# Kernel optimization log

Hardware: AMD Instinct MI355X
Metric: run time of the kernel (lower is better)

The kernel has to match this reference:

```python
import jax, jax.numpy as jnp
import numpy as np

TOP_K = 25
END_K = 25
TEMP = 0.07
CON_RATE = 0.1
NUM_LABELS = 2
NEG_INF = -1e30  # stand-in for -inf that keeps softmax/topk well-behaved


def _l2norm(x):
    return x / jnp.sqrt(jnp.sum(x * x, axis=-1, keepdims=True))


def _head(x, dense_w, dense_b, out_w, out_b):
    # dropout is identity in eval mode
    h = jnp.tanh(x @ dense_w + dense_b)
    return h @ out_w + out_b


def _ce(logits, targets):
    lp = jax.nn.log_softmax(logits, axis=-1)
    return -jnp.take_along_axis(lp, targets[:, None], axis=1).mean()


def setup_inputs() -> dict:
    key = jax.random.key(0)
    ks = jax.random.split(key, 10)
    B, K, H = 128, 32768, 768
    fq = jax.random.normal(ks[2], (K, H), dtype=jnp.float32)
    # buffer init in torch: F.normalize(feature_queue, dim=0)
    fq = fq / jnp.linalg.norm(fq, axis=0, keepdims=True)
    s = 0.02
    return {
        "pooled": jax.random.normal(ks[0], (B, H), dtype=jnp.float32),
        "labels": jax.random.randint(ks[1], (B,), 0, NUM_LABELS),
        "feature_queue": fq,
        "label_queue": jax.random.randint(ks[3], (K,), 0, NUM_LABELS),
        "cls_dense_w": s * jax.random.normal(ks[4], (H, H), dtype=jnp.float32),
        "cls_dense_b": jnp.zeros((H,), jnp.float32),
        "cls_out_w": s * jax.random.normal(ks[5], (H, NUM_LABELS), dtype=jnp.float32),
        "cls_out_b": jnp.zeros((NUM_LABELS,), jnp.float32),
        "con_dense_w": s * jax.random.normal(ks[6], (H, H), dtype=jnp.float32),
        "con_dense_b": jnp.zeros((H,), jnp.float32),
        "con_out_w": s * jax.random.normal(ks[7], (H, H), dtype=jnp.float32),
        "con_out_b": jnp.zeros((H,), jnp.float32),
    }


def _select_pos_neg(liner_q, labels, feature_queue, label_queue, pos_min, neg_min):
    # cos_sim: [B, K]  (einsum 'nc,kc->nk'; queue rows are detached)
    cos_sim = jnp.einsum("nc,kc->nk", liner_q, feature_queue)
    pos_mask = labels[:, None] == label_queue[None, :]  # [B, K] bool
    pos_sample = jnp.where(pos_mask, cos_sim, NEG_INF)
    neg_sample = jnp.where(pos_mask, NEG_INF, cos_sim)
    pos_top, _ = jax.lax.top_k(pos_sample, pos_min)   # [B, pos_min]
    neg_top, _ = jax.lax.top_k(neg_sample, neg_min)   # [B, neg_min]
    pos = jnp.concatenate([pos_top[:, :TOP_K], pos_top[:, -END_K:]], axis=-1)
    pos = pos.reshape(-1, 1)                                   # [B*(TOP_K+END_K), 1]
    neg = jnp.tile(neg_top, (1, TOP_K + END_K)).reshape(-1, neg_min)
    return jnp.concatenate([pos, neg], axis=-1) / TEMP


def reference(pooled, labels, feature_queue, label_queue,
              cls_dense_w, cls_dense_b, cls_out_w, cls_out_b,
              con_dense_w, con_dense_b, con_out_w, con_out_b):
    # data-dependent top-k sizes (concrete int labels -> static sizes)
    pm = np.asarray(labels)[:, None] == np.asarray(label_queue)[None, :]
    pos_min = int(pm.sum(-1).min())
    neg_min = int((~pm).sum(-1).min())

    logits_cls = _head(pooled, cls_dense_w, cls_dense_b, cls_out_w, cls_out_b)
    loss_cls = _ce(logits_cls, labels)

    liner_q = _l2norm(_head(pooled, con_dense_w, con_dense_b, con_out_w, con_out_b))
    logits_con = _select_pos_neg(liner_q, labels, jax.lax.stop_gradient(feature_queue),
                                 label_queue, pos_min, neg_min)
    labels_con = jnp.zeros((logits_con.shape[0],), jnp.int32)
    loss_con = _ce(logits_con, labels_con)

    loss = loss_con * CON_RATE + loss_cls * (1.0 - CON_RATE)
    return loss
```

## Files before the change

### kernel.cpp

```cpp
#include <hip/hip_runtime.h>
#include <math.h>

#define BB 128
#define HH 768
#define KQ 32768
#define PCAP 18432
#define NB 4096
#define CCAP 512

constexpr float TINV = 1.0f / 0.07f;

typedef __attribute__((ext_vector_type(8))) short short8;
typedef __attribute__((ext_vector_type(4))) float f32x4;
typedef __attribute__((address_space(3))) void lds_void;
typedef const __attribute__((address_space(1))) void gbl_void;

__device__ __forceinline__ unsigned short f2bf(float f) {
  unsigned u = __float_as_uint(f);
  unsigned r = u + 0x7FFFu + ((u >> 16) & 1u);
  return (unsigned short)(r >> 16);
}
__device__ __forceinline__ float bf2f(unsigned short h) {
  return __uint_as_float(((unsigned)h) << 16);
}
__device__ __forceinline__ unsigned cvtpk(float a, float b) {
  unsigned r;
  asm("v_cvt_pk_bf16_f32 %0, %1, %2" : "=v"(r) : "v"(a), "v"(b));
  return r;
}
__device__ __forceinline__ unsigned f2key(float f) {
  unsigned u = __float_as_uint(f);
  return u ^ (unsigned)(((int)u >> 31) | 0x80000000);
}
__device__ __forceinline__ float key2f(unsigned k) {
  unsigned u = (k & 0x80000000u) ? (k & 0x7FFFFFFFu) : ~k;
  return __uint_as_float(u);
}
__device__ __forceinline__ unsigned long long shfl_down_u64(unsigned long long v, int o) {
  unsigned lo = (unsigned)v, hi = (unsigned)(v >> 32);
  lo = __shfl_down(lo, o);
  hi = __shfl_down(hi, o);
  return ((unsigned long long)hi << 32) | lo;
}
__device__ __forceinline__ void gl16(const unsigned short* g, unsigned short* l) {
  __builtin_amdgcn_global_load_lds((gbl_void*)g, (lds_void*)l, 16, 0, 0);
}

__global__ __launch_bounds__(256) void prep_kernel(
    const float* __restrict__ W0, const float* __restrict__ W1,
    const float* __restrict__ W2, const float* __restrict__ pooled,
    unsigned short* __restrict__ Wt0, unsigned short* __restrict__ Wt1,
    unsigned short* __restrict__ Wt2, unsigned short* __restrict__ pooledb,
    float* __restrict__ out) {
  const int bid = blockIdx.x, tid = threadIdx.x;
  if (bid == 0 && tid == 0) out[0] = 0.0f;
  if (bid < 432) {
    const float* W = (bid < 144) ? W0 : (bid < 288 ? W1 : W2);
    unsigned short* Wt = (bid < 144) ? Wt0 : (bid < 288 ? Wt1 : Wt2);
    const int t = bid % 144;
    const int k0 = (t / 12) * 64, n0 = (t % 12) * 64;
    __shared__ float Ls[64][65];
    const int r = tid >> 4, c4 = (tid & 15) * 4;
#pragma unroll
    for (int i = 0; i < 4; ++i) {
      const int rr = r + i * 16;
      const float4 v = *reinterpret_cast<const float4*>(W + (size_t)(k0 + rr) * HH + n0 + c4);
      Ls[rr][c4 + 0] = v.x; Ls[rr][c4 + 1] = v.y;
      Ls[rr][c4 + 2] = v.z; Ls[rr][c4 + 3] = v.w;
    }
    __syncthreads();
#pragma unroll
    for (int i = 0; i < 4; ++i) {
      const int rn = r + i * 16;
      ushort4 o;
      o.x = f2bf(Ls[c4 + 0][rn]);
      o.y = f2bf(Ls[c4 + 1][rn]);
      o.z = f2bf(Ls[c4 + 2][rn]);
      o.w = f2bf(Ls[c4 + 3][rn]);
      *reinterpret_cast<ushort4*>(Wt + (size_t)(n0 + rn) * HH + k0 + c4) = o;
    }
  } else {
    const int idx = (bid - 432) * 1024 + tid * 4;
    const float4 v = *reinterpret_cast<const float4*>(pooled + idx);
    ushort4 o;
    o.x = f2bf(v.x); o.y = f2bf(v.y); o.z = f2bf(v.z); o.w = f2bf(v.w);
    *reinterpret_cast<ushort4*>(pooledb + idx) = o;
  }
}

__device__ __forceinline__ void head_core(
    unsigned short (*Abuf)[128 * 64], const unsigned short* __restrict__ Ab,
    const unsigned short* __restrict__ Wt, const float* __restrict__ bias,
    unsigned short* __restrict__ Out, bool do_tanh, int q0, int tid) {
  const int lane = tid & 63, wid = tid >> 6;
  const int a_r = lane & 15, a_kq = lane >> 4;
  int asrc[4], adst[4];
#pragma unroll
  for (int j = 0; j < 4; ++j) {
    const int rr = (wid * 4 + j) * 8 + (lane >> 3);
    const int kb = (lane & 7) ^ (rr & 7);
    asrc[j] = rr * HH + kb * 8;
    adst[j] = (wid * 4 + j) * 512;
  }
  const int bn = q0 + wid * 16 + a_r;
  const unsigned short* __restrict__ bptr = Wt + (size_t)bn * HH + a_kq * 8;
  int aslot[2];
#pragma unroll
  for (int st = 0; st < 2; ++st) aslot[st] = (((st * 4 + a_kq) ^ (a_r & 7)) << 3);

  f32x4 acc[8];
#pragma unroll
  for (int m = 0; m < 8; ++m) acc[m] = (f32x4){0.f, 0.f, 0.f, 0.f};

#pragma unroll
  for (int j = 0; j < 4; ++j) gl16(Ab + asrc[j], &Abuf[0][adst[j]]);
  __builtin_amdgcn_sched_barrier(0);
#pragma unroll
  for (int j = 0; j < 4; ++j) gl16(Ab + 64 + asrc[j], &Abuf[1][adst[j]]);
  __builtin_amdgcn_sched_barrier(0);
  short8 bv[4];
#pragma unroll
  for (int p = 0; p < 4; ++p)
    bv[p] = *reinterpret_cast<const short8*>(bptr + p * 32);
  __builtin_amdgcn_sched_barrier(0);
  asm volatile("s_waitcnt vmcnt(8)" ::: "memory");
  __builtin_amdgcn_s_barrier();
  __builtin_amdgcn_sched_barrier(0);

#pragma unroll
  for (int c = 0; c < 12; ++c) {
    if (c + 2 < 12) {
#pragma unroll
      for (int j = 0; j < 4; ++j)
        gl16(Ab + (c + 2) * 64 + asrc[j], &Abuf[(c + 2) % 3][adst[j]]);
    }
    __builtin_amdgcn_sched_barrier(0);
    const unsigned short* __restrict__ Abc = Abuf[c % 3];
#pragma unroll
    for (int st = 0; st < 2; ++st) {
      const int s = c * 2 + st;
      const short8 bb = bv[s & 3];
      if (s + 4 < 24)
        bv[s & 3] = *reinterpret_cast<const short8*>(bptr + (s + 4) * 32);
      const int sl = aslot[st];
#pragma unroll
      for (int m = 0; m < 8; ++m) {
        const short8 aa =
            *reinterpret_cast<const short8*>(&Abc[(m * 16 + a_r) * 64 + sl]);
        acc[m] = __builtin_amdgcn_mfma_f32_16x16x32_bf16(aa, bb, acc[m], 0, 0, 0);
      }
    }
    if (c < 11) {
      __builtin_amdgcn_sched_barrier(0);
      if (c == 0)       asm volatile("s_waitcnt vmcnt(10)" ::: "memory");
      else if (c <= 9)  asm volatile("s_waitcnt vmcnt(8)" ::: "memory");
      else              asm volatile("s_waitcnt vmcnt(2)" ::: "memory");
      __builtin_amdgcn_s_barrier();
      __builtin_amdgcn_sched_barrier(0);
    }
  }

  const float bvl = bias[bn];
#pragma unroll
  for (int m = 0; m < 8; ++m)
#pragma unroll
    for (int r = 0; r < 4; ++r) {
      float v = acc[m][r] + bvl;
      if (do_tanh) v = tanhf(v);
      Out[(size_t)(m * 16 + a_kq * 4 + r) * HH + bn] = f2bf(v);
    }
}

__global__ __launch_bounds__(256) void heads_mfma(
    const unsigned short* __restrict__ pooledb,
    const unsigned short* __restrict__ Wt0, const float* __restrict__ b0,
    unsigned short* __restrict__ H1b,
    const unsigned short* __restrict__ Wt1, const float* __restrict__ b1,
    unsigned short* __restrict__ H2b) {
  __shared__ unsigned short Abuf[3][128 * 64];
  const int z = blockIdx.x / 12;
  const int q0 = (blockIdx.x % 12) * 64;
  head_core(Abuf, pooledb, z ? Wt1 : Wt0, z ? b1 : b0, z ? H2b : H1b, true, q0,
            threadIdx.x);
}

__global__ __launch_bounds__(256) void out_gemm(
    const unsigned short* __restrict__ H2b, const unsigned short* __restrict__ Wt2,
    const float* __restrict__ b2v, unsigned short* __restrict__ Yb) {
  __shared__ unsigned short Abuf[3][128 * 64];
  head_core(Abuf, H2b, Wt2, b2v, Yb, false, blockIdx.x * 64, threadIdx.x);
}

__global__ __launch_bounds__(256, 2) void cos_gemm_mfma(
    const unsigned short* __restrict__ qh, const float* __restrict__ FQ,
    unsigned short* __restrict__ Cb) {
  __shared__ unsigned short Abuf[4][128 * 64];
  const int tid = threadIdx.x;
  const int lane = tid & 63, wid = tid >> 6;
  const int bid = blockIdx.x;
  const int swz = (bid & 7) * 64 + (bid >> 3);
  const int q0 = swz * 64;
  const int a_r = lane & 15, a_kq = lane >> 4;

  int asrc[4], adst[4];
#pragma unroll
  for (int j = 0; j < 4; ++j) {
    const int rr = (wid * 4 + j) * 8 + (lane >> 3);
    const int kb = (lane & 7) ^ (rr & 7);
    asrc[j] = rr * HH + kb * 8;
    adst[j] = (wid * 4 + j) * 512;
  }
  const float* __restrict__ bptr = FQ + (size_t)(q0 + wid * 16 + a_r) * HH + a_kq * 8;
  int aslot[2];
#pragma unroll
  for (int st = 0; st < 2; ++st) aslot[st] = (((st * 4 + a_kq) ^ (a_r & 7)) << 3);

  f32x4 acc[8];
#pragma unroll
  for (int m = 0; m < 8; ++m) acc[m] = (f32x4){0.f, 0.f, 0.f, 0.f};

#pragma unroll
  for (int j = 0; j < 4; ++j) gl16(qh + asrc[j], &Abuf[0][adst[j]]);
  __builtin_amdgcn_sched_barrier(0);
#pragma unroll
  for (int j = 0; j < 4; ++j) gl16(qh + 64 + asrc[j], &Abuf[1][adst[j]]);
  __builtin_amdgcn_sched_barrier(0);
#pragma unroll
  for (int j = 0; j < 4; ++j) gl16(qh + 128 + asrc[j], &Abuf[2][adst[j]]);
  __builtin_amdgcn_sched_barrier(0);
  float4 bv[8][2];
#pragma unroll
  for (int p = 0; p < 8; ++p) {
    bv[p][0] = *reinterpret_cast<const float4*>(bptr + p * 32);
    bv[p][1] = *reinterpret_cast<const float4*>(bptr + p * 32 + 4);
  }
  __builtin_amdgcn_sched_barrier(0);
  asm volatile("s_waitcnt vmcnt(24)" ::: "memory");
  __builtin_amdgcn_s_barrier();
  __builtin_amdgcn_sched_barrier(0);

#pragma unroll
  for (int c = 0; c < 12; ++c) {
    if (c + 3 < 12) {
#pragma unroll
      for (int j = 0; j < 4; ++j)
        gl16(qh + (c + 3) * 64 + asrc[j], &Abuf[(c + 3) & 3][adst[j]]);
    }
    __builtin_amdgcn_sched_barrier(0);
    const unsigned short* __restrict__ Ab = Abuf[c & 3];
#pragma unroll
    for (int st = 0; st < 2; ++st) {
      const int s = c * 2 + st;
      const float4 v0 = bv[s & 7][0], v1 = bv[s & 7][1];
      if (s + 8 < 24) {
        bv[s & 7][0] = *reinterpret_cast<const float4*>(bptr + (s + 8) * 32);
        bv[s & 7][1] = *reinterpret_cast<const float4*>(bptr + (s + 8) * 32 + 4);
      }
      union { short8 s8; unsigned u[4]; } cb;
      cb.u[0] = cvtpk(v0.x, v0.y);
      cb.u[1] = cvtpk(v0.z, v0.w);
      cb.u[2] = cvtpk(v1.x, v1.y);
      cb.u[3] = cvtpk(v1.z, v1.w);
      const short8 bb = cb.s8;
      const int sl = aslot[st];
#pragma unroll
      for (int m = 0; m < 8; ++m) {
        const short8 aa =
            *reinterpret_cast<const short8*>(&Ab[(m * 16 + a_r) * 64 + sl]);
        acc[m] = __builtin_amdgcn_mfma_f32_16x16x32_bf16(aa, bb, acc[m], 0, 0, 0);
      }
    }
    if (c < 11) {
      __builtin_amdgcn_sched_barrier(0);
      if (c == 0)      asm volatile("s_waitcnt vmcnt(28)" ::: "memory");
      else if (c == 1) asm volatile("s_waitcnt vmcnt(32)" ::: "memory");
      else if (c <= 7) asm volatile("s_waitcnt vmcnt(20)" ::: "memory");
      else if (c == 8) asm volatile("s_waitcnt vmcnt(16)" ::: "memory");
      else if (c == 9) asm volatile("s_waitcnt vmcnt(8)" ::: "memory");
      else             asm volatile("s_waitcnt vmcnt(0)" ::: "memory");
      __builtin_amdgcn_s_barrier();
      __builtin_amdgcn_sched_barrier(0);
    }
  }

  const int ccol = q0 + wid * 16 + a_r;
#pragma unroll
  for (int m = 0; m < 8; ++m)
#pragma unroll
    for (int r = 0; r < 4; ++r)
      Cb[(size_t)(m * 16 + a_kq * 4 + r) * KQ + ccol] = f2bf(acc[m][r]);
}

__global__ __launch_bounds__(1024) void select_kernel(
    const unsigned short* __restrict__ Cb, const unsigned short* __restrict__ Yb,
    const unsigned short* __restrict__ H1b, const float* __restrict__ W2,
    const float* __restrict__ cb2, const int* __restrict__ labels,
    const int* __restrict__ lq, float* __restrict__ out) {
  const int b = blockIdx.x;
  const int tid = threadIdx.x;
  const int lane = tid & 63, wid = tid >> 6;
  const unsigned short* __restrict__ row = Cb + (size_t)b * KQ;
  const int lab = labels[b];

  __shared__ __align__(16) unsigned poskeys[PCAP];
  __shared__ unsigned hist[NB + 1];
  __shared__ unsigned cand[3][CCAP];
  __shared__ int candn[3];
  __shared__ float redm[16], reds[16], redmin[16], redmax[16];
  __shared__ int redn[16];
  __shared__ unsigned wsum[16];
  __shared__ float shc0[16], shc1[16];
  __shared__ int abin[3], acnt[3];
  __shared__ unsigned akey[3];
  __shared__ unsigned long long accg;
  __shared__ float gs0, gsm, s_logE, s_vmin, s_vmax, s_rs;
  __shared__ float ssq[2];
  __shared__ int s_cnt, s_m, has01;

  if (tid == 0) { s_cnt = 0; gs0 = 0.f; gsm = 0.f; accg = 0ull; has01 = 0; }
  if (tid < 3) candn[tid] = 0;

  float cp0 = 0.f, cp1 = 0.f;
  if (tid < HH) {
    const float v = bf2f(H1b[(size_t)b * HH + tid]);
    cp0 = v * W2[tid * 2 + 0];
    cp1 = v * W2[tid * 2 + 1];
  }
#pragma unroll
  for (int o = 32; o; o >>= 1) {
    cp0 += __shfl_down(cp0, o);
    cp1 += __shfl_down(cp1, o);
  }
  if (lane == 0) { shc0[wid] = cp0; shc1[wid] = cp1; }

  float ssl = 0.f;
  if (tid < 96) {
    const short8 y8 =
        *reinterpret_cast<const short8*>(Yb + (size_t)b * HH + tid * 8);
#pragma unroll
    for (int e = 0; e < 8; ++e) {
      const float v = bf2f((unsigned short)y8[e]);
      ssl = fmaf(v, v, ssl);
    }
  }
#pragma unroll
  for (int o = 32; o; o >>= 1) ssl += __shfl_down(ssl, o);
  if (lane == 0 && wid < 2) ssq[wid] = ssl;
  __syncthreads();
  if (tid == 0) s_rs = rsqrtf(ssq[0] + ssq[1]);
  __syncthreads();
  const float rs = s_rs;

  const int base = tid << 5;
  unsigned qm = 0u;
  {
    const int4* __restrict__ lq4 = reinterpret_cast<const int4*>(lq + base);
#pragma unroll
    for (int u = 0; u < 8; ++u) {
      const int4 q = lq4[u];
      qm |= (unsigned)(q.x != 0) << (u * 4 + 0);
      qm |= (unsigned)(q.y != 0) << (u * 4 + 1);
      qm |= (unsigned)(q.z != 0) << (u * 4 + 2);
      qm |= (unsigned)(q.w != 0) << (u * 4 + 3);
    }
  }
  if (tid < BB) atomicOr(&has01, 1 << labels[tid]);
  const unsigned pmask = lab ? qm : ~qm;
  float va[32];
#pragma unroll
  for (int u = 0; u < 4; ++u) {
    const short8 y8 = *reinterpret_cast<const short8*>(row + base + (u << 3));
#pragma unroll
    for (int e = 0; e < 8; ++e)
      va[(u << 3) + e] = bf2f((unsigned short)y8[e]) * rs;
  }
  float mneg = -3.0e38f, sneg = 0.f, vmin = 3.0e38f, vmax = -3.0e38f;
#pragma unroll
  for (int j = 0; j < 32; ++j) {
    if ((pmask >> j) & 1u) {
      vmin = fminf(vmin, va[j]);
      vmax = fmaxf(vmax, va[j]);
    } else {
      mneg = fmaxf(mneg, va[j] * TINV);
    }
  }
#pragma unroll
  for (int j = 0; j < 32; ++j) {
    if (!((pmask >> j) & 1u)) sneg += __expf(va[j] * TINV - mneg);
  }
  int nc = __popc(qm);
#pragma unroll
  for (int o = 32; o; o >>= 1) {
    const float mo = __shfl_down(mneg, o), so = __shfl_down(sneg, o);
    const float M = fmaxf(mneg, mo);
    sneg = sneg * __expf(mneg - M) + so * __expf(mo - M);
    mneg = M;
    vmin = fminf(vmin, __shfl_down(vmin, o));
    vmax = fmaxf(vmax, __shfl_down(vmax, o));
    nc += __shfl_down(nc, o);
  }
  if (lane == 0) {
    redm[wid] = mneg; reds[wid] = sneg; redmin[wid] = vmin; redmax[wid] = vmax;
    redn[wid] = nc;
  }

  const int np = __popc(pmask);
  unsigned incl = (unsigned)np;
#pragma unroll
  for (int o = 1; o < 64; o <<= 1) {
    const unsigned t = __shfl_up(incl, o);
    if (lane >= o) incl += t;
  }
  const unsigned excl = incl - (unsigned)np;
  const unsigned wtot = __shfl(incl, 63);
  unsigned wbase = 0u;
  if (lane == 63) wbase = (unsigned)atomicAdd(&s_cnt, (int)wtot);
  wbase = __shfl(wbase, 63);
  const int ofs = (int)(wbase + excl);
  if (ofs + np <= PCAP) {
#pragma unroll
    for (int j = 0; j < 32; ++j) {
      if ((pmask >> j) & 1u)
        poskeys[ofs + __popc(pmask & ((1u << j) - 1u))] = f2key(va[j]);
    }
  }
  __syncthreads();

  const int P = s_cnt;
  if (tid == 0) {
    float M = redm[0], S = 0.f;
    float mn = redmin[0], mx = redmax[0];
    int n1 = 0;
    for (int w = 1; w < 16; ++w) {
      M = fmaxf(M, redm[w]);
      mn = fminf(mn, redmin[w]);
      mx = fmaxf(mx, redmax[w]);
    }
    for (int w = 0; w < 16; ++w) { S += reds[w] * __expf(redm[w] - M); n1 += redn[w]; }
    s_logE = M + logf(S);
    s_vmin = mn;
    s_vmax = mx;
    int mm = 0x7fffffff;
    if (has01 & 1) mm = min(mm, KQ - n1);
    if (has01 & 2) mm = min(mm, n1);
    s_m = mm;
  }
  if (tid < ((4 - (P & 3)) & 3)) poskeys[P + tid] = 0u;
  for (int i = tid; i < NB + 1; i += 1024) hist[i] = 0u;
  __syncthreads();

  const float cE = s_logE;
  const int m = s_m;
  const float vmn = s_vmin;
  const float scale = (float)NB * (1.0f - 1e-6f) / fmaxf(s_vmax - vmn, 1e-30f);
  auto key2bin = [&](unsigned k) {
    int bn = (int)((key2f(k) - vmn) * scale);
    return bn < 0 ? 0 : (bn > NB - 1 ? NB - 1 : bn);
  };

  for (int i = tid; i < P; i += 1024) atomicAdd(&hist[key2bin(poskeys[i])], 1u);
  __syncthreads();

  const int t4 = tid << 2;
  const unsigned h0 = hist[t4], h1 = hist[t4 + 1], h2 = hist[t4 + 2], h3 = hist[t4 + 3];
  const unsigned part = h0 + h1 + h2 + h3;
  unsigned sinc = part;
#pragma unroll
  for (int o = 1; o < 64; o <<= 1) {
    const unsigned t = __shfl_up(sinc, o);
    if (lane >= o) sinc += t;
  }
  if (lane == 63) wsum[wid] = sinc;
  __syncthreads();
  unsigned woff = 0;
  for (int w = 0; w < wid; ++w) woff += wsum[w];
  const unsigned exb = woff + sinc - part;
  hist[t4] = exb; hist[t4 + 1] = exb + h0; hist[t4 + 2] = exb + h0 + h1;
  hist[t4 + 3] = exb + h0 + h1 + h2;
  if (tid == 1023) hist[NB] = exb + part;
  __syncthreads();

  const int rt0 = 25, rt1 = m - 25, rt2 = m;
  const unsigned idx0 = (unsigned)(P - rt0), idx1 = (unsigned)(P - rt1), idx2 = (unsigned)(P - rt2);
#pragma unroll
  for (int i = 0; i < 4; ++i) {
    const int bb = t4 + i;
    const unsigned pb = hist[bb], pb1 = hist[bb + 1];
    if (pb <= idx0 && idx0 < pb1) { abin[0] = bb; acnt[0] = P - (int)pb1; }
    if (pb <= idx1 && idx1 < pb1) { abin[1] = bb; acnt[1] = P - (int)pb1; }
    if (pb <= idx2 && idx2 < pb1) { abin[2] = bb; acnt[2] = P - (int)pb1; }
  }
  __syncthreads();

  const int tb0 = abin[0], tb1 = abin[1], tb2 = abin[2];
  for (int i = tid; i < P; i += 1024) {
    const unsigned k = poskeys[i];
    const int bn = key2bin(k);
    if (bn == tb0) { const int p = atomicAdd(&candn[0], 1); if (p < CCAP) cand[0][p] = k; }
    if (bn == tb1) { const int p = atomicAdd(&candn[1], 1); if (p < CCAP) cand[1][p] = k; }
    if (bn == tb2) { const int p = atomicAdd(&candn[2], 1); if (p < CCAP) cand[2][p] = k; }
  }
  __syncthreads();

  if (wid < 3) {
    const int j = wid;
    const int rts[3] = {rt0, rt1, rt2};
    const int cnt = candn[j] < CCAP ? candn[j] : CCAP;
    const int rr = rts[j] - acnt[j];
    for (int i = lane; i < cnt; i += 64) {
      const unsigned k = cand[j][i];
      int gt = 0, eq = 0;
      for (int q = 0; q < cnt; ++q) {
        const unsigned kq = cand[j][q];
        gt += (kq > k);
        eq += (kq == k);
      }
      if (gt < rr && rr <= gt + eq) akey[j] = k;
    }
  }
  __syncthreads();

  const unsigned a0 = akey[0], a1 = akey[1], a2 = akey[2];
  const int P4c = (P + 3) >> 2;
  const uint4* __restrict__ pk4 = reinterpret_cast<const uint4*>(poskeys);

  float s0 = 0.f, sm = 0.f;
  unsigned q0c = 0, q1c = 0, q2c = 0;
  for (int i = tid; i < P4c; i += 1024) {
    const uint4 kv = pk4[i];
    const unsigned ks[4] = {kv.x, kv.y, kv.z, kv.w};
#pragma unroll
    for (int j = 0; j < 4; ++j) {
      const unsigned k = ks[j];
      if (k > a2) {
        ++q2c;
        const bool top = (k > a0), mid = (k <= a1);
        if (k > a1) ++q1c;
        if (top) ++q0c;
        if (top || mid) {
          const float a = key2f(k) * TINV;
          const float d = cE - a;
          const float fv = fmaxf(d, 0.f) + log1pf(__expf(-fabsf(d)));
          if (top) s0 += fv;
          if (mid) sm += fv;
        }
      }
    }
  }
  unsigned long long pc = (unsigned long long)q0c |
                          ((unsigned long long)q1c << 20) |
                          ((unsigned long long)q2c << 40);
#pragma unroll
  for (int o = 32; o; o >>= 1) {
    s0 += __shfl_down(s0, o);
    sm += __shfl_down(sm, o);
    pc += shfl_down_u64(pc, o);
  }
  if (lane == 0) {
    atomicAdd(&gs0, s0);
    atomicAdd(&gsm, sm);
    atomicAdd(&accg, pc);
  }
  __syncthreads();
  if (tid == 0) {
    const unsigned long long t = accg;
    const float C0 = (float)(unsigned)(t & 0xFFFFFu);
    const float C1 = (float)(unsigned)((t >> 20) & 0xFFFFFu);
    const float C2 = (float)(unsigned)((t >> 40) & 0xFFFFFu);
    auto fval = [&](unsigned kk) {
      const float a = key2f(kk) * TINV;
      const float d = cE - a;
      return fmaxf(d, 0.f) + log1pf(__expf(-fabsf(d)));
    };
    const float f0 = fval(a0), f1 = fval(a1), f2 = fval(a2);
    const float top25 = gs0 + (25.0f - C0) * f0;
    const float mid = gsm + ((float)m - C2) * f2 - ((float)(m - 25) - C1) * f1;
    float l0 = cb2[0], l1 = cb2[1];
    for (int w = 0; w < 16; ++w) { l0 += shc0[w]; l1 += shc1[w]; }
    const float mx = fmaxf(l0, l1), mn = fminf(l0, l1);
    const float lse = mx + log1pf(__expf(mn - mx));
    const float ce = lse - (lab ? l1 : l0);
    atomicAdd(out, 0.9f * ce * (1.0f / 128.0f) +
                       0.1f * (top25 + mid) * (1.0f / 6400.0f));
  }
}

extern "C" void kernel_launch(void* const* d_in, const int* in_sizes, int n_in,
                              void* d_out, int out_size, void* d_ws, size_t ws_size,
                              hipStream_t stream) {
  const float* pooled = (const float*)d_in[0];
  const int* labels = (const int*)d_in[1];
  const float* fq = (const float*)d_in[2];
  const int* lq = (const int*)d_in[3];
  const float* cls_dw = (const float*)d_in[4];
  const float* cls_db = (const float*)d_in[5];
  const float* cls_ow = (const float*)d_in[6];
  const float* cls_ob = (const float*)d_in[7];
  const float* con_dw = (const float*)d_in[8];
  const float* con_db = (const float*)d_in[9];
  const float* con_ow = (const float*)d_in[10];
  const float* con_ob = (const float*)d_in[11];
  float* out = (float*)d_out;

  float* ws = (float*)d_ws;
  unsigned short* Cb = (unsigned short*)ws;
  unsigned short* Yb = Cb + (size_t)BB * KQ;
  unsigned short* H1b = Yb + 98304;
  unsigned short* H2b = H1b + 98304;
  unsigned short* pooledb = H2b + 98304;
  unsigned short* Wt0 = Cb;
  unsigned short* Wt1 = Wt0 + 589824;
  unsigned short* Wt2 = Wt1 + 589824;

  prep_kernel<<<528, 256, 0, stream>>>(cls_dw, con_dw, con_ow, pooled,
                                       Wt0, Wt1, Wt2, pooledb, out);
  heads_mfma<<<24, 256, 0, stream>>>(pooledb, Wt0, cls_db, H1b,
                                     Wt1, con_db, H2b);
  out_gemm<<<12, 256, 0, stream>>>(H2b, Wt2, con_ob, Yb);
  cos_gemm_mfma<<<512, 256, 0, stream>>>(Yb, fq, Cb);
  select_kernel<<<128, 1024, 0, stream>>>(Cb, Yb, H1b, cls_ow, cls_ob,
                                          labels, lq, out);
}
```

Before: 81.57 us.

## Retile head GEMMs to 64x128 tiles with full-K LDS preload

```diff
diff --git a/kernel.cpp b/kernel.cpp
--- a/kernel.cpp
+++ b/kernel.cpp
@@ -88,87 +88,70 @@
   }
 }
 
-__device__ __forceinline__ void head_core(
-    unsigned short (*Abuf)[128 * 64], const unsigned short* __restrict__ Ab,
+__device__ __forceinline__ void head2_core(
+    unsigned short (*Al)[64 * 64], const unsigned short* __restrict__ A,
     const unsigned short* __restrict__ Wt, const float* __restrict__ bias,
-    unsigned short* __restrict__ Out, bool do_tanh, int q0, int tid) {
+    unsigned short* __restrict__ Out, bool do_tanh, int r0, int n0, int tid) {
   const int lane = tid & 63, wid = tid >> 6;
   const int a_r = lane & 15, a_kq = lane >> 4;
-  int asrc[4], adst[4];
-#pragma unroll
-  for (int j = 0; j < 4; ++j) {
-    const int rr = (wid * 4 + j) * 8 + (lane >> 3);
+
+  int asrc[2], adst[2];
+#pragma unroll
+  for (int j = 0; j < 2; ++j) {
+    const int rr = wid * 16 + j * 8 + (lane >> 3);
     const int kb = (lane & 7) ^ (rr & 7);
-    asrc[j] = rr * HH + kb * 8;
-    adst[j] = (wid * 4 + j) * 512;
-  }
-  const int bn = q0 + wid * 16 + a_r;
-  const unsigned short* __restrict__ bptr = Wt + (size_t)bn * HH + a_kq * 8;
+    asrc[j] = (r0 + rr) * HH + kb * 8;
+    adst[j] = (wid * 16 + j * 8) * 64;
+  }
+#pragma unroll
+  for (int c = 0; c < 12; ++c)
+#pragma unroll
+    for (int j = 0; j < 2; ++j)
+      gl16(A + c * 64 + asrc[j], &Al[c][adst[j]]);
+  asm volatile("s_waitcnt vmcnt(0)" ::: "memory");
+  __builtin_amdgcn_s_barrier();
+
+  const unsigned short* __restrict__ bp0 =
+      Wt + (size_t)(n0 + wid * 32 + a_r) * HH + a_kq * 8;
+  const unsigned short* __restrict__ bp1 = bp0 + (size_t)16 * HH;
   int aslot[2];
 #pragma unroll
   for (int st = 0; st < 2; ++st) aslot[st] = (((st * 4 + a_kq) ^ (a_r & 7)) << 3);
 
-  f32x4 acc[8];
-#pragma unroll
-  for (int m = 0; m < 8; ++m) acc[m] = (f32x4){0.f, 0.f, 0.f, 0.f};
-
-#pragma unroll
-  for (int j = 0; j < 4; ++j) gl16(Ab + asrc[j], &Abuf[0][adst[j]]);
-  __builtin_amdgcn_sched_barrier(0);
-#pragma unroll
-  for (int j = 0; j < 4; ++j) gl16(Ab + 64 + asrc[j], &Abuf[1][adst[j]]);
-  __builtin_amdgcn_sched_barrier(0);
-  short8 bv[4];
-#pragma unroll
-  for (int p = 0; p < 4; ++p)
-    bv[p] = *reinterpret_cast<const short8*>(bptr + p * 32);
-  __builtin_amdgcn_sched_barrier(0);
-  asm volatile("s_waitcnt vmcnt(8)" ::: "memory");
-  __builtin_amdgcn_s_barrier();
-  __builtin_amdgcn_sched_barrier(0);
-
-#pragma unroll
-  for (int c = 0; c < 12; ++c) {
-    if (c + 2 < 12) {
-#pragma unroll
-      for (int j = 0; j < 4; ++j)
-        gl16(Ab + (c + 2) * 64 + asrc[j], &Abuf[(c + 2) % 3][adst[j]]);
-    }
-    __builtin_amdgcn_sched_barrier(0);
-    const unsigned short* __restrict__ Abc = Abuf[c % 3];
-#pragma unroll
-    for (int st = 0; st < 2; ++st) {
-      const int s = c * 2 + st;
-      const short8 bb = bv[s & 3];
-      if (s + 4 < 24)
-        bv[s & 3] = *reinterpret_cast<const short8*>(bptr + (s + 4) * 32);
-      const int sl = aslot[st];
-#pragma unroll
-      for (int m = 0; m < 8; ++m) {
-        const short8 aa =
-            *reinterpret_cast<const short8*>(&Abc[(m * 16 + a_r) * 64 + sl]);
-        acc[m] = __builtin_amdgcn_mfma_f32_16x16x32_bf16(aa, bb, acc[m], 0, 0, 0);
+  f32x4 acc[4][2];
+#pragma unroll
+  for (int m = 0; m < 4; ++m)
+#pragma unroll
+    for (int n = 0; n < 2; ++n) acc[m][n] = (f32x4){0.f, 0.f, 0.f, 0.f};
+
+#pragma unroll
+  for (int s = 0; s < 24; ++s) {
+    const short8 b0 = *reinterpret_cast<const short8*>(bp0 + s * 32);
+    const short8 b1 = *reinterpret_cast<const short8*>(bp1 + s * 32);
+    const int c = s >> 1;
+    const int sl = aslot[s & 1];
+#pragma unroll
+    for (int m = 0; m < 4; ++m) {
+      const short8 aa =
+          *reinterpret_cast<const short8*>(&Al[c][(m * 16 + a_r) * 64 + sl]);
+      acc[m][0] = __builtin_amdgcn_mfma_f32_16x16x32_bf16(aa, b0, acc[m][0], 0, 0, 0);
+      acc[m][1] = __builtin_amdgcn_mfma_f32_16x16x32_bf16(aa, b1, acc[m][1], 0, 0, 0);
+    }
+  }
+
+#pragma unroll
+  for (int n = 0; n < 2; ++n) {
+    const int col = n0 + wid * 32 + n * 16 + a_r;
+    const float bvl = bias[col];
+#pragma unroll
+    for (int m = 0; m < 4; ++m)
+#pragma unroll
+      for (int r = 0; r < 4; ++r) {
+        float v = acc[m][n][r] + bvl;
+        if (do_tanh) v = tanhf(v);
+        Out[(size_t)(r0 + m * 16 + a_kq * 4 + r) * HH + col] = f2bf(v);
       }
-    }
-    if (c < 11) {
-      __builtin_amdgcn_sched_barrier(0);
-      if (c == 0)       asm volatile("s_waitcnt vmcnt(10)" ::: "memory");
-      else if (c <= 9)  asm volatile("s_waitcnt vmcnt(8)" ::: "memory");
-      else              asm volatile("s_waitcnt vmcnt(2)" ::: "memory");
-      __builtin_amdgcn_s_barrier();
-      __builtin_amdgcn_sched_barrier(0);
-    }
-  }
-
-  const float bvl = bias[bn];
-#pragma unroll
-  for (int m = 0; m < 8; ++m)
-#pragma unroll
-    for (int r = 0; r < 4; ++r) {
-      float v = acc[m][r] + bvl;
-      if (do_tanh) v = tanhf(v);
-      Out[(size_t)(m * 16 + a_kq * 4 + r) * HH + bn] = f2bf(v);
-    }
+  }
 }
 
 __global__ __launch_bounds__(256) void heads_mfma(
@@ -177,18 +160,18 @@
     unsigned short* __restrict__ H1b,
     const unsigned short* __restrict__ Wt1, const float* __restrict__ b1,
     unsigned short* __restrict__ H2b) {
-  __shared__ unsigned short Abuf[3][128 * 64];
-  const int z = blockIdx.x / 12;
-  const int q0 = (blockIdx.x % 12) * 64;
-  head_core(Abuf, pooledb, z ? Wt1 : Wt0, z ? b1 : b0, z ? H2b : H1b, true, q0,
-            threadIdx.x);
+  __shared__ unsigned short Al[12][64 * 64];
+  const int z = blockIdx.z;
+  head2_core(Al, pooledb, z ? Wt1 : Wt0, z ? b1 : b0, z ? H2b : H1b, true,
+             blockIdx.y * 64, blockIdx.x * 128, threadIdx.x);
 }
 
 __global__ __launch_bounds__(256) void out_gemm(
     const unsigned short* __restrict__ H2b, const unsigned short* __restrict__ Wt2,
     const float* __restrict__ b2v, unsigned short* __restrict__ Yb) {
-  __shared__ unsigned short Abuf[3][128 * 64];
-  head_core(Abuf, H2b, Wt2, b2v, Yb, false, blockIdx.x * 64, threadIdx.x);
+  __shared__ unsigned short Al[12][64 * 64];
+  head2_core(Al, H2b, Wt2, b2v, Yb, false, blockIdx.y * 64, blockIdx.x * 128,
+             threadIdx.x);
 }
 
 __global__ __launch_bounds__(256, 2) void cos_gemm_mfma(
@@ -614,9 +597,9 @@
 
   prep_kernel<<<528, 256, 0, stream>>>(cls_dw, con_dw, con_ow, pooled,
                                        Wt0, Wt1, Wt2, pooledb, out);
-  heads_mfma<<<24, 256, 0, stream>>>(pooledb, Wt0, cls_db, H1b,
-                                     Wt1, con_db, H2b);
-  out_gemm<<<12, 256, 0, stream>>>(H2b, Wt2, con_ob, Yb);
+  heads_mfma<<<dim3(6, 2, 2), 256, 0, stream>>>(pooledb, Wt0, cls_db, H1b,
+                                                Wt1, con_db, H2b);
+  out_gemm<<<dim3(6, 2), 256, 0, stream>>>(H2b, Wt2, con_ob, Yb);
   cos_gemm_mfma<<<512, 256, 0, stream>>>(Yb, fq, Cb);
   select_kernel<<<128, 1024, 0, stream>>>(Cb, Yb, H1b, cls_ow, cls_ob,
                                           labels, lq, out);
```

After: 80.34 us. No clear change (-1.5%).
